# Kernel optimization log

Hardware: AMD Instinct MI355X
Metric: run time of the kernel (lower is better)

## Reference

```python
import jax, jax.numpy as jnp
from jax import lax
import numpy as np

B, T, F = 4, 16000, 512          # batch, frames, enc_num_feats
NB = 24                          # 3 stacks x 8 layers
DILS = [2 ** l for _ in range(3) for l in range(8)]


def _prelu(x, a):
    return jnp.where(x >= 0, x, a * x)


def _conv(x, w, stride=1, pad=0, dil=1, groups=1):
    # x: [B,C,T], w: [O, C//groups, K]
    return lax.conv_general_dilated(x, w, (stride,), [(pad, pad)], rhs_dilation=(dil,),
                                    dimension_numbers=('NCH', 'OIH', 'NCH'),
                                    feature_group_count=groups)


def _tconv(x, w, stride=1):
    # torch ConvTranspose1d, weight layout [in, out, k], padding=0
    k = w.shape[-1]
    wf = jnp.flip(w, -1).transpose(1, 0, 2)  # [out, in, k]
    return lax.conv_general_dilated(x, wf, (1,), [(k - 1, k - 1)], lhs_dilation=(stride,),
                                    dimension_numbers=('NCH', 'OIH', 'NCH'))


def _pw(x, w, b):
    # 1x1 conv as GEMM; w: [O,C], b: [O]
    return jnp.einsum('oc,bct->bot', w, x) + b[:, None]


def _branch(x, p):
    # encoder
    f = _conv(x, p['enc_w0'], stride=8)                       # [B,512,1999]
    f = _prelu(_conv(f, p['enc_w1']), p['enc_a'][0])          # [B,512,1997]
    f = _prelu(_conv(f, p['enc_w2']), p['enc_a'][1])          # [B,512,1995]
    # mask generator (TCN)
    o = _pw(f, p['mg_in_w'], p['mg_in_b'])                    # [B,128,t]
    for i in range(NB):
        d = DILS[i]
        h = _prelu(_pw(o, p['blk_w1'][i], p['blk_b1'][i]), p['blk_a1'][i])     # [B,32,t]
        h = _conv(h, p['blk_dw'][i][:, None, :], pad=d, dil=d, groups=32) + p['blk_db'][i][:, None]
        h = _prelu(h, p['blk_a2'][i])
        if i < NB - 1:  # last block has no residual path
            o = o + _pw(h, p['blk_rw'][i], p['blk_rb'][i])
        o = o + _pw(h, p['blk_sw'][i], p['blk_sb'][i])
    m = jax.nn.sigmoid(_pw(_prelu(o, p['mg_out_a']), p['mg_out_w'], p['mg_out_b']))  # [B,1024,t]
    b, _, t = f.shape
    m = m.reshape(b, 2, F, t)
    y = (m * f[:, None]).reshape(b * 2, F, t)
    # decoder
    y = _prelu(_tconv(y, p['dec_w1']), p['dec_a'][0])
    y = _prelu(_tconv(y, p['dec_w2']), p['dec_a'][1])
    y = _tconv(y, p['dec_w3'], stride=8)                      # [2B,1,T]
    return y.reshape(b, 2, -1)


_NAMES = ['x_real', 'x_imag', 'enc_w0', 'enc_w1', 'enc_w2', 'enc_a', 'mg_in_w', 'mg_in_b',
          'blk_w1', 'blk_b1', 'blk_a1', 'blk_dw', 'blk_db', 'blk_a2', 'blk_rw', 'blk_rb',
          'blk_sw', 'blk_sb', 'mg_out_a', 'mg_out_w', 'mg_out_b', 'dec_w1', 'dec_w2', 'dec_a', 'dec_w3']


def _forward(*args):
    p = dict(zip(_NAMES, args))
    out_r = _branch(p['x_real'], p)
    out_i = _branch(p['x_imag'], p)
    return jnp.stack([out_r, out_i])  # [2, B, 2, T]; axis0 = (real, imag)


def setup_inputs() -> dict:
    key = jax.random.key(0)
    ks = jax.random.split(key, 16)
    n = lambda k, s, sc: jax.random.normal(k, s, dtype=jnp.float32) * sc
    f32 = jnp.float32
    return {
        'x_real': jax.random.normal(ks[0], (B, 1, T), dtype=f32),
        'x_imag': jax.random.normal(ks[1], (B, 1, T), dtype=f32),
        'enc_w0': n(ks[2], (512, 1, 16), 0.1),
        'enc_w1': n(ks[3], (512, 512, 3), 0.03),
        'enc_w2': n(ks[4], (512, 512, 3), 0.03),
        'enc_a': jnp.full((2,), 0.25, f32),
        'mg_in_w': n(ks[5], (128, 512), 0.05),
        'mg_in_b': jnp.zeros((128,), f32),
        'blk_w1': n(ks[6], (NB, 32, 128), 0.08),
        'blk_b1': jnp.zeros((NB, 32), f32),
        'blk_a1': jnp.full((NB,), 0.25, f32),
        'blk_dw': n(ks[7], (NB, 32, 3), 0.2),
        'blk_db': jnp.zeros((NB, 32), f32),
        'blk_a2': jnp.full((NB,), 0.25, f32),
        'blk_rw': n(ks[8], (NB, 128, 32), 0.08),  # index NB-1 unused (no_residual)
        'blk_rb': jnp.zeros((NB, 128), f32),
        'blk_sw': n(ks[9], (NB, 128, 32), 0.08),
        'blk_sb': jnp.zeros((NB, 128), f32),
        'mg_out_a': jnp.asarray(0.25, f32),
        'mg_out_w': n(ks[10], (1024, 128), 0.08),
        'mg_out_b': jnp.zeros((1024,), f32),
        'dec_w1': n(ks[11], (512, 512, 3), 0.03),
        'dec_w2': n(ks[12], (512, 512, 3), 0.03),
        'dec_a': jnp.full((2,), 0.25, f32),
        'dec_w3': n(ks[13], (512, 1, 16), 0.1),
    }


def reference(x_real, x_imag, enc_w0, enc_w1, enc_w2, enc_a, mg_in_w, mg_in_b,
              blk_w1, blk_b1, blk_a1, blk_dw, blk_db, blk_a2, blk_rw, blk_rb,
              blk_sw, blk_sb, mg_out_a, mg_out_w, mg_out_b, dec_w1, dec_w2, dec_a, dec_w3):
    return _forward(x_real, x_imag, enc_w0, enc_w1, enc_w2, enc_a, mg_in_w, mg_in_b,
                    blk_w1, blk_b1, blk_a1, blk_dw, blk_db, blk_a2, blk_rw, blk_rb,
                    blk_sw, blk_sb, mg_out_a, mg_out_w, mg_out_b, dec_w1, dec_w2, dec_a, dec_w3)
```

## Files before the change

kernel.cpp:

```cpp
#include <hip/hip_runtime.h>
#include <hip/hip_cooperative_groups.h>

namespace cg = cooperative_groups;


typedef unsigned short u16;
typedef __attribute__((ext_vector_type(8))) short bf16x8_t;
typedef __attribute__((ext_vector_type(4))) float f32x4_t;

#define ST    2064
#define HALO  8
#define TR    2064
#define RHALO 8

#define U_F0H   0ULL
#define U_F1H   8454144ULL
#define F_F2    8454144ULL
#define F_D2    0ULL
#define U_YH    33816576ULL
#define U_D1H   50724864ULL
#define F_O     33816576ULL
#define F_G0    35930112ULL
#define F_G1    36458496ULL
#define F_W     36986880ULL
#define W_MGIN  0ULL
#define W_MGOUT 65536ULL
#define W_W1T   196608ULL
#define W_WSUMT 294912ULL
#define W_BSUM  393216ULL
#define U_WB    74766336ULL
#define F_FLAG  38956032ULL
#define F_G2    38964224ULL
#define F_G3    39492608ULL
#define U_MKB   74104832ULL
#define U_W1B   74375168ULL
#define U_WSB   74563584ULL

#define WS_HI 0
#define WS_LO 5120
#define W1_HI 10240
#define W1_LO 14592
#define OB_HI 0
#define OB_LO 8704
#define HB_HI 0
#define HB_LO 2560

__device__ __forceinline__ float prelu_f(float x, float a) { return x >= 0.f ? x : a * x; }
__device__ __forceinline__ u16 f2b(float f) {
    unsigned u = __float_as_uint(f);
    return (u16)((u + 0x7FFF + ((u >> 16) & 1)) >> 16);
}
__device__ __forceinline__ float b2f(u16 h) {
    return __uint_as_float((unsigned)h << 16);
}
__device__ __forceinline__ void gload16(const void* g, void* l) {
    __builtin_amdgcn_global_load_lds(
        (const __attribute__((address_space(1))) unsigned*)g,
        (__attribute__((address_space(3))) unsigned*)l, 16, 0, 0);
}

__global__ __launch_bounds__(256) void prep_all(
    const float* __restrict__ ew1, const float* __restrict__ ew2,
    const float* __restrict__ dw1, const float* __restrict__ dw2,
    const float* __restrict__ mgin_w, const float* __restrict__ mgout_w,
    const float* __restrict__ bw1, const float* __restrict__ brw,
    const float* __restrict__ brb, const float* __restrict__ bsw,
    const float* __restrict__ bsb, float* __restrict__ wsf, u16* __restrict__ wsb,
    unsigned* __restrict__ flags)
{
    const int task = blockIdx.y;
    const int idx  = blockIdx.x * 256 + threadIdx.x;
    const int stride = gridDim.x * 256;
    if (task < 4) {
        const float* src = (task == 0) ? ew1 : (task == 1) ? ew2 : (task == 2) ? dw1 : dw2;
        u16* dst = wsb + U_WB + (size_t)task * 786432ULL;
        const bool dec = (task >= 2);
        for (int n = idx; n < 786432; n += stride) {
            int j = n >> 18, o = (n >> 9) & 511, c = n & 511;
            float v = dec ? src[(size_t)c * 1536 + o * 3 + (2 - j)]
                          : src[(size_t)o * 1536 + c * 3 + j];
            dst[n] = f2b(v);
        }
    } else if (task == 4) {
        float* dst = wsf + F_W + W_MGIN;
        for (int n = idx; n < 65536; n += stride) {
            int o = n & 127, c = n >> 7;
            dst[n] = mgin_w[(size_t)o * 512 + c];
        }
    } else if (task == 5) {
        u16* dst = wsb + U_MKB;
        for (int n = idx; n < 262144; n += stride) {
            int C = n & 127, m = (n >> 7) & 1023, p = n >> 17;
            float v = mgout_w[(size_t)m * 128 + C];
            u16 hh = f2b(v);
            if (p) hh = f2b(v - b2f(hh));
            dst[n] = hh;
        }
    } else if (task == 6) {
        float* dstf = wsf + F_W + W_W1T;
        for (int n = idx; n < 4096; n += stride) {
            int cc = n & 31, C = n >> 5;
            dstf[n] = bw1[(size_t)cc * 128 + C];
        }
        u16* dstb = wsb + U_W1B;
        for (int n = idx; n < 188416; n += stride) {
            int C = n & 127, cgi = (n >> 7) & 31, p = (n >> 12) & 1, ii = n >> 13;
            float v = bw1[(size_t)(ii + 1) * 4096 + cgi * 128 + C];
            u16 hh = f2b(v);
            if (p) hh = f2b(v - b2f(hh));
            dstb[n] = hh;
        }
    } else if (task == 7) {
        u16* dst = wsb + U_WSB;
        for (int n = idx; n < 196608; n += stride) {
            int cc = n & 31, C = (n >> 5) & 127, p = (n >> 12) & 1, i = n >> 13;
            float v = bsw[(size_t)i * 4096 + C * 32 + cc];
            if (i < 23) v += brw[(size_t)i * 4096 + C * 32 + cc];
            u16 hh = f2b(v);
            if (p) hh = f2b(v - b2f(hh));
            dst[n] = hh;
        }
    } else if (task == 8) {
        float* dst = wsf + F_W + W_BSUM;
        for (int n = idx; n < 3072; n += stride) {
            int i = n >> 7;
            float v = bsb[n];
            if (i < 23) v += brb[n];
            dst[n] = v;
        }
    } else if (task == 9) {
        const unsigned long long uoff[4] = { U_F0H, U_F1H, U_YH, U_D1H };
        const int nbArr[4]   = { 8, 8, 16, 16 };
        const int trArr[4]   = { 1999, 1997, 1995, 1997 };
#pragma unroll
        for (int z = 0; z < 4; z++) {
            unsigned* base = (unsigned*)(wsb + uoff[z]);
            const int nb = nbArr[z], Treal = trArr[z];
            const int prcnt = TR - Treal;
            const int total = nb * prcnt * 256;
            for (int n = idx; n < total; n += stride) {
                const int col = n & 255;
                const int r   = n >> 8;
                const int bb  = r / prcnt;
                const int pr  = r % prcnt;
                const int row = (pr < RHALO) ? pr : (Treal + pr);
                base[((size_t)bb * TR + row) * 256 + col] = 0u;
            }
        }
    } else {
        for (int n = idx; n < 4096; n += stride) flags[n] = 0u;
    }
}

__global__ __launch_bounds__(256) void enc0_kernel(
    const float* __restrict__ xr, const float* __restrict__ xi,
    const float* __restrict__ w0, u16* __restrict__ f0h)
{
    const int t  = blockIdx.x * 256 + threadIdx.x;
    const int c0 = blockIdx.y * 8;
    const int b  = blockIdx.z;
    if (t >= 1999) return;
    const float* x = (b < 4) ? (xr + (size_t)b * 16000) : (xi + (size_t)(b - 4) * 16000);
    float xv[16];
    const int base = t * 8;
#pragma unroll
    for (int k = 0; k < 16; k++) xv[k] = x[base + k];
    union { u16 u[8]; uint4 v; } p;
#pragma unroll
    for (int cq = 0; cq < 8; cq++) {
        const float* w = w0 + (size_t)(c0 + cq) * 16;
        float acc = 0.f;
#pragma unroll
        for (int k = 0; k < 16; k++) acc = fmaf(xv[k], w[k], acc);
        p.u[cq] = f2b(acc);
    }
    *(uint4*)&f0h[((size_t)b * TR + RHALO + t) * 512 + c0] = p.v;
}

template <int JOFF, int OUTF32>
__global__ __launch_bounds__(256) void conv_mfma(
    const u16* __restrict__ in, u16* __restrict__ out16, float* __restrict__ out32,
    const u16* __restrict__ wM, const float* __restrict__ alpha_p, int Tout)
{
    __shared__ __align__(16) u16 smem[17408];
    u16* As = smem;
    u16* Bs = smem + 12288;
    const int tid  = threadIdx.x;
    const int t0   = blockIdx.x * 128;
    const int ob   = blockIdx.y * 128;
    const int b    = blockIdx.z;
    const int l15  = tid & 15;
    const int quad = (tid >> 4) & 3;
    const int wave = tid >> 6;
    const int wm   = (wave & 1) * 64;
    const int wn   = (wave >> 1) * 64;
    const u16* inb = in + (size_t)b * TR * 512;
    const int wvb  = wave * 1024;

    f32x4_t acc[4][4];
#pragma unroll
    for (int i = 0; i < 4; i++)
#pragma unroll
        for (int k = 0; k < 4; k++) acc[i][k] = (f32x4_t){0.f, 0.f, 0.f, 0.f};

    for (int c0 = 0; c0 < 512; c0 += 32) {
#pragma unroll
        for (int k = 0; k < 6; k++) {
            const int v = k * 256 + tid;
            const int j = v >> 9, r = (v >> 2) & 127, c = v & 3;
            const int cg = c ^ ((r >> 1) & 3);
            gload16(&wM[((size_t)(j * 512 + ob + r)) * 512 + c0 + cg * 8],
                    (char*)As + k * 4096 + wvb);
        }
#pragma unroll
        for (int k = 0; k < 2; k++) {
            const int v = k * 256 + tid;
            const int r = v >> 2, c = v & 3;
            const int cg = c ^ ((r >> 1) & 3);
            gload16(&inb[(size_t)(RHALO + t0 + JOFF + r) * 512 + c0 + cg * 8],
                    (char*)Bs + k * 4096 + wvb);
        }
        if (tid < 16) {
            const int v = 512 + tid;
            const int r = v >> 2, c = v & 3;
            const int cg = c ^ ((r >> 1) & 3);
            gload16(&inb[(size_t)(RHALO + t0 + JOFF + r) * 512 + c0 + cg * 8],
                    (char*)Bs + 8192);
        }
        __syncthreads();
#pragma unroll
        for (int j = 0; j < 3; j++) {
            bf16x8_t aw[4], bi[4];
#pragma unroll
            for (int mf = 0; mf < 4; mf++) {
                const int row = wm + mf * 16 + l15;
                const int ch  = quad ^ ((row >> 1) & 3);
                aw[mf] = *(const bf16x8_t*)&As[j * 4096 + row * 32 + ch * 8];
            }
#pragma unroll
            for (int nf = 0; nf < 4; nf++) {
                const int row = wn + nf * 16 + l15 + j;
                const int ch  = quad ^ ((row >> 1) & 3);
                bi[nf] = *(const bf16x8_t*)&Bs[row * 32 + ch * 8];
            }
#pragma unroll
            for (int mf = 0; mf < 4; mf++)
#pragma unroll
                for (int nf = 0; nf < 4; nf++) {
                    if (OUTF32)
                        acc[mf][nf] = __builtin_amdgcn_mfma_f32_16x16x32_bf16(
                            bi[nf], aw[mf], acc[mf][nf], 0, 0, 0);
                    else
                        acc[mf][nf] = __builtin_amdgcn_mfma_f32_16x16x32_bf16(
                            aw[mf], bi[nf], acc[mf][nf], 0, 0, 0);
                }
        }
        __syncthreads();
    }

    const float alpha = *alpha_p;
    if (!OUTF32) {
        u16* tile = smem;
#pragma unroll
        for (int mf = 0; mf < 4; mf++)
#pragma unroll
            for (int nf = 0; nf < 4; nf++) {
                const int t_loc = wn + nf * 16 + l15;
                const int c_loc = wm + mf * 16 + quad * 4;
                f32x4_t a = acc[mf][nf];
                ushort4 s;
                s.x = f2b(prelu_f(a.x, alpha));
                s.y = f2b(prelu_f(a.y, alpha));
                s.z = f2b(prelu_f(a.z, alpha));
                s.w = f2b(prelu_f(a.w, alpha));
                *(ushort4*)&tile[t_loc * 136 + c_loc] = s;
            }
        __syncthreads();
        for (int v = tid; v < 2048; v += 256) {
            const int row = v >> 4, seg = v & 15;
            const int t = t0 + row;
            if (t < Tout)
                *(uint4*)&out16[((size_t)b * TR + RHALO + t) * 512 + ob + seg * 8] =
                    *(const uint4*)&tile[row * 136 + seg * 8];
        }
    } else {
#pragma unroll
        for (int mf = 0; mf < 4; mf++)
#pragma unroll
            for (int nf = 0; nf < 4; nf++) {
                const int o  = ob + wm + mf * 16 + l15;
                const int tb = t0 + wn + nf * 16 + quad * 4;
                f32x4_t a = acc[mf][nf];
                float v0 = prelu_f(a.x, alpha), v1 = prelu_f(a.y, alpha);
                float v2 = prelu_f(a.z, alpha), v3 = prelu_f(a.w, alpha);
                float* p = out32 + ((size_t)(b * 512 + o)) * ST + HALO + tb;
                if (tb + 3 < Tout) {
                    *(float4*)p = make_float4(v0, v1, v2, v3);
                } else {
                    if (tb + 0 < Tout) p[0] = v0;
                    if (tb + 1 < Tout) p[1] = v1;
                    if (tb + 2 < Tout) p[2] = v2;
                    if (tb + 3 < Tout) p[3] = v3;
                }
            }
    }
}

__global__ __launch_bounds__(256) void mgin_kernel(
    const float* __restrict__ f2, float* __restrict__ o_buf, float* __restrict__ g_out,
    const float* __restrict__ wT, const float* __restrict__ bias,
    const float* __restrict__ w1T0, const float* __restrict__ b1_0,
    const float* __restrict__ a1_0)
{
    __shared__ float Bs[16][64];
    __shared__ float As[16][128];
    __shared__ float o_lds[128][64];
    const int tid = threadIdx.x;
    const int t0  = blockIdx.x * 64;
    const int b   = blockIdx.y;
    const float* f2b_ = f2 + (size_t)b * 512 * ST + HALO + t0;

    float acc[8][4];
#pragma unroll
    for (int i = 0; i < 8; i++)
#pragma unroll
        for (int k = 0; k < 4; k++) acc[i][k] = 0.f;
    const int tx = tid & 15, ty = tid >> 4;

    for (int c0 = 0; c0 < 512; c0 += 16) {
        {
            int c = tid >> 4, p = tid & 15;
            *(float4*)(&Bs[c][p * 4]) = *(const float4*)(f2b_ + (size_t)(c0 + c) * ST + p * 4);
        }
#pragma unroll
        for (int r = 0; r < 2; r++) {
            int n4 = tid + r * 256;
            int c = n4 >> 5, m4 = n4 & 31;
            *(float4*)(&As[c][m4 * 4]) = *(const float4*)(wT + (size_t)(c0 + c) * 128 + m4 * 4);
        }
        __syncthreads();
#pragma unroll 2
        for (int c = 0; c < 16; c++) {
            float4 bv = *(const float4*)(&Bs[c][tx * 4]);
            float a[8];
            *(float4*)(&a[0]) = *(const float4*)(&As[c][ty * 8]);
            *(float4*)(&a[4]) = *(const float4*)(&As[c][ty * 8 + 4]);
#pragma unroll
            for (int oi = 0; oi < 8; oi++) {
                acc[oi][0] = fmaf(a[oi], bv.x, acc[oi][0]);
                acc[oi][1] = fmaf(a[oi], bv.y, acc[oi][1]);
                acc[oi][2] = fmaf(a[oi], bv.z, acc[oi][2]);
                acc[oi][3] = fmaf(a[oi], bv.w, acc[oi][3]);
            }
        }
        __syncthreads();
    }

    const int tb = t0 + tx * 4;
#pragma unroll
    for (int oi = 0; oi < 8; oi++) {
        const int o = ty * 8 + oi;
        const float bo = bias[o];
        float vv[4];
#pragma unroll
        for (int kk = 0; kk < 4; kk++) vv[kk] = acc[oi][kk] + bo;
        *(float4*)(&o_lds[o][tx * 4]) = make_float4(vv[0], vv[1], vv[2], vv[3]);
        float* orow = o_buf + (size_t)(b * 128 + o) * ST + HALO + tb;
        if (tb + 3 < 1995) {
            *(float4*)orow = make_float4(vv[0], vv[1], vv[2], vv[3]);
        } else {
#pragma unroll
            for (int kk = 0; kk < 4; kk++)
                if (tb + kk < 1995) orow[kk] = vv[kk];
        }
    }
    __syncthreads();

    const int t = tid & 63, cg_ = tid >> 6;
    const float a1 = *a1_0;
    float acc2[8];
#pragma unroll
    for (int q = 0; q < 8; q++) acc2[q] = b1_0[cg_ * 8 + q];
    for (int C = 0; C < 128; C++) {
        const float ov = o_lds[C][t];
        const float4* wr = (const float4*)(w1T0 + (size_t)C * 32 + cg_ * 8);
        float4 w0 = wr[0], w1 = wr[1];
        acc2[0] = fmaf(w0.x, ov, acc2[0]); acc2[1] = fmaf(w0.y, ov, acc2[1]);
        acc2[2] = fmaf(w0.z, ov, acc2[2]); acc2[3] = fmaf(w0.w, ov, acc2[3]);
        acc2[4] = fmaf(w1.x, ov, acc2[4]); acc2[5] = fmaf(w1.y, ov, acc2[5]);
        acc2[6] = fmaf(w1.z, ov, acc2[6]); acc2[7] = fmaf(w1.w, ov, acc2[7]);
    }
    const int tt = t0 + t;
    if (tt < 1995) {
#pragma unroll
        for (int q = 0; q < 8; q++)
            g_out[(size_t)(b * 32 + cg_ * 8 + q) * ST + HALO + tt] = prelu_f(acc2[q], a1);
    }
}

__device__ __forceinline__ void poll_acquire(const unsigned* flags, int b, int j,
                                             int k, unsigned target)
{
    int lo = j - k; if (lo < 0) lo = 0;
    int hi = j + k; if (hi > 31) hi = 31;
    for (int n = lo; n <= hi; n++) {
        if (n == j) continue;
        const unsigned* p = flags + ((b << 5) + n) * 16;
        while (__hip_atomic_load(p, __ATOMIC_RELAXED, __HIP_MEMORY_SCOPE_AGENT) < target)
            __builtin_amdgcn_s_sleep(2);
    }
    __builtin_amdgcn_fence(__ATOMIC_ACQUIRE, "agent");
}

__device__ __forceinline__ void store_pair_agent(float* dst, int trel, float v0, float v1)
{
    if (trel + 1 < 1995) {
        unsigned long long raw =
            ((unsigned long long)__float_as_uint(v1) << 32) | __float_as_uint(v0);
        __hip_atomic_store((unsigned long long*)dst, raw,
                           __ATOMIC_RELAXED, __HIP_MEMORY_SCOPE_AGENT);
    } else if (trel < 1995) {
        __hip_atomic_store(dst, v0, __ATOMIC_RELAXED, __HIP_MEMORY_SCOPE_AGENT);
    }
}

__global__ __launch_bounds__(512) void tcn_fused(
    float* __restrict__ g0, float* __restrict__ g1,
    float* __restrict__ g2, float* __restrict__ g3,
    float* __restrict__ o_buf,
    const float* __restrict__ dw_all, const float* __restrict__ db_all,
    const float* __restrict__ a2_all,
    const u16* __restrict__ wsb16, const float* __restrict__ bsum_all,
    const u16* __restrict__ w1b16, const float* __restrict__ b1_all,
    const float* __restrict__ a1_all, unsigned* __restrict__ wflag)
{
    __shared__ __align__(16) u16  wbuf[18944];
    __shared__ __align__(16) u16  hbuf[5120];
    __shared__ __align__(16) u16  ob16[17408];
    __shared__ __align__(16) float g_lds[2][2176];
    __shared__ __align__(16) float halo_lds[8320];

    const int tid = threadIdx.x;
    const int blk = blockIdx.x;
    const int b   = blk & 7;
    const int jt  = blk >> 3;
    const int t0  = jt * 64;
    float* gbuf[4] = { g0, g1, g2, g3 };

    const int wv   = tid >> 6;
    const int l15  = tid & 15;
    const int quad = (tid >> 4) & 3;
    const int Cb   = wv * 16 + quad * 4;

    f32x4_t o_acc[4];
#pragma unroll
    for (int k = 0; k < 4; k++)
#pragma unroll
        for (int r = 0; r < 4; r++)
            o_acc[k][r] = o_buf[((size_t)(b * 128 + Cb + r)) * ST + HALO + t0 + k * 16 + l15];
    {
        int cc = tid >> 4, seg = tid & 15;
        *(float4*)&g_lds[0][cc * 68 + seg * 4] =
            *(const float4*)&g0[((size_t)(b * 32 + cc)) * ST + HALO + t0 + seg * 4];
    }

    for (int i = 0; i < 24; i++) {
        const int dil  = 1 << (i & 7);
        const int dil2 = (dil < 2) ? 2 : dil;
        const int k_rd = (dil > 64) ? 2 : 1;
        const float* gin_g = gbuf[i & 3];
        float* gout_g      = gbuf[(i + 1) & 3];
        float* gin_lds  = g_lds[i & 1];
        float* gout_lds = g_lds[(i + 1) & 1];

        {
            const u16* wsg = wsb16 + (size_t)i * 8192;
#pragma unroll
            for (int k = 0; k < 2; k++) {
                int c = tid + k * 512;
                int p = c >> 9, r = (c >> 2) & 127, s = c & 3;
                *(uint4*)&wbuf[(p ? WS_LO : WS_HI) + r * 40 + s * 8] =
                    *(const uint4*)&wsg[c * 8];
            }
            if (i < 23) {
                const u16* w1g = w1b16 + (size_t)i * 8192;
#pragma unroll
                for (int k = 0; k < 2; k++) {
                    int c = tid + k * 512;
                    int p = c >> 9, cgi = (c >> 4) & 31, s = c & 15;
                    *(uint4*)&wbuf[(p ? W1_LO : W1_HI) + cgi * 136 + s * 8] =
                        *(const uint4*)&w1g[c * 8];
                }
            }
        }

        if (i > 0 && tid == 0) poll_acquire(wflag, b, jt, k_rd, (unsigned)i);
        __syncthreads();

        {
            const int dsh = (dil2 >= 128) ? 7 : (dil2 >= 64) ? 6 : (dil2 >= 32) ? 5
                          : (dil2 >= 16) ? 4 : (dil2 >= 8) ? 3 : (dil2 >= 4) ? 2 : 1;
            const int total = 32 << dsh;
            for (int n = tid; n < total; n += 512) {
                const int cc = n >> dsh;
                const int pi = n & (dil2 - 1);
                const int hc = pi * 2;
                const int tg = (hc < dil2) ? (t0 - dil2 + hc) : (t0 + 64 + hc - dil2);
                float v0 = 0.f, v1 = 0.f;
                const float* src = gin_g + ((size_t)(b * 32 + cc)) * ST + HALO + tg;
                if (tg >= 0 && tg + 1 < 1995) {
                    unsigned long long raw = __hip_atomic_load(
                        (const unsigned long long*)src,
                        __ATOMIC_RELAXED, __HIP_MEMORY_SCOPE_AGENT);
                    v0 = __uint_as_float((unsigned)raw);
                    v1 = __uint_as_float((unsigned)(raw >> 32));
                } else {
                    if (tg >= 0 && tg < 1995)
                        v0 = __hip_atomic_load(src, __ATOMIC_RELAXED,
                                               __HIP_MEMORY_SCOPE_AGENT);
                    if (tg + 1 >= 0 && tg + 1 < 1995)
                        v1 = __hip_atomic_load(src + 1, __ATOMIC_RELAXED,
                                               __HIP_MEMORY_SCOPE_AGENT);
                }
                halo_lds[cc * 260 + hc]     = v0;
                halo_lds[cc * 260 + hc + 1] = v1;
            }
        }
        __syncthreads();

        {
            const float a2 = a2_all[i];
            const int t = tid & 63, cc0 = (tid >> 6) * 4;
            const int tt = t0 + t;
            ushort4 hi4, lo4;
            u16 hs[4], ls[4];
#pragma unroll
            for (int q = 0; q < 4; q++) {
                const int cc = cc0 + q;
                const float w0 = dw_all[i * 96 + cc * 3 + 0];
                const float w1v = dw_all[i * 96 + cc * 3 + 1];
                const float w2 = dw_all[i * 96 + cc * 3 + 2];
                const float ctr = gin_lds[cc * 68 + t];
                float lo = 0.f, hi = 0.f;
                const int tm = tt - dil;
                if (tm >= 0)
                    lo = (tm >= t0) ? gin_lds[cc * 68 + (tm - t0)]
                                    : halo_lds[cc * 260 + (tm - t0 + dil2)];
                const int tp = tt + dil;
                if (tp < 1995)
                    hi = (tp < t0 + 64) ? gin_lds[cc * 68 + (tp - t0)]
                                        : halo_lds[cc * 260 + (dil2 + tp - t0 - 64)];
                float s = db_all[i * 32 + cc] + w1v * ctr;
                s = fmaf(w0, lo, s);
                s = fmaf(w2, hi, s);
                const float hval = prelu_f(s, a2);
                const u16 hh = f2b(hval);
                hs[q] = hh;
                ls[q] = f2b(hval - b2f(hh));
            }
            hi4.x = hs[0]; hi4.y = hs[1]; hi4.z = hs[2]; hi4.w = hs[3];
            lo4.x = ls[0]; lo4.y = ls[1]; lo4.z = ls[2]; lo4.w = ls[3];
            *(ushort4*)&hbuf[HB_HI + t * 40 + cc0] = hi4;
            *(ushort4*)&hbuf[HB_LO + t * 40 + cc0] = lo4;
        }
        __syncthreads();

        {
            const bf16x8_t a_hi = *(const bf16x8_t*)&wbuf[WS_HI + (wv * 16 + l15) * 40 + quad * 8];
            const bf16x8_t a_lo = *(const bf16x8_t*)&wbuf[WS_LO + (wv * 16 + l15) * 40 + quad * 8];
            const float4 bs4 = *(const float4*)&bsum_all[i * 128 + Cb];
#pragma unroll
            for (int k = 0; k < 4; k++) {
                const bf16x8_t b_hi = *(const bf16x8_t*)&hbuf[HB_HI + (k * 16 + l15) * 40 + quad * 8];
                const bf16x8_t b_lo = *(const bf16x8_t*)&hbuf[HB_LO + (k * 16 + l15) * 40 + quad * 8];
                f32x4_t acc = o_acc[k];
                acc = __builtin_amdgcn_mfma_f32_16x16x32_bf16(a_lo, b_hi, acc, 0, 0, 0);
                acc = __builtin_amdgcn_mfma_f32_16x16x32_bf16(a_hi, b_lo, acc, 0, 0, 0);
                acc = __builtin_amdgcn_mfma_f32_16x16x32_bf16(a_hi, b_hi, acc, 0, 0, 0);
                acc.x += bs4.x; acc.y += bs4.y; acc.z += bs4.z; acc.w += bs4.w;
                o_acc[k] = acc;
            }
        }

        if (i == 23) break;

#pragma unroll
        for (int k = 0; k < 4; k++) {
            ushort4 hi4, lo4;
            u16 hs[4], ls[4];
#pragma unroll
            for (int r = 0; r < 4; r++) {
                const float v = o_acc[k][r];
                const u16 hh = f2b(v);
                hs[r] = hh;
                ls[r] = f2b(v - b2f(hh));
            }
            hi4.x = hs[0]; hi4.y = hs[1]; hi4.z = hs[2]; hi4.w = hs[3];
            lo4.x = ls[0]; lo4.y = ls[1]; lo4.z = ls[2]; lo4.w = ls[3];
            const int t_loc = k * 16 + l15;
            *(ushort4*)&ob16[OB_HI + t_loc * 136 + Cb] = hi4;
            *(ushort4*)&ob16[OB_LO + t_loc * 136 + Cb] = lo4;
        }
        __syncthreads();

        {
            const int cgb = (wv & 1) * 16;
            const int tb  = (wv >> 1) * 16;
            const float4 b14 = *(const float4*)&b1_all[(i + 1) * 32 + cgb + quad * 4];
            f32x4_t ga = (f32x4_t){b14.x, b14.y, b14.z, b14.w};
            f32x4_t gc = (f32x4_t){0.f, 0.f, 0.f, 0.f};
#pragma unroll
            for (int slab = 0; slab < 4; slab++) {
                const bf16x8_t wa_hi = *(const bf16x8_t*)&wbuf[W1_HI + (cgb + l15) * 136 + slab * 32 + quad * 8];
                const bf16x8_t wa_lo = *(const bf16x8_t*)&wbuf[W1_LO + (cgb + l15) * 136 + slab * 32 + quad * 8];
                const bf16x8_t obh   = *(const bf16x8_t*)&ob16[OB_HI + (tb + l15) * 136 + slab * 32 + quad * 8];
                const bf16x8_t obl   = *(const bf16x8_t*)&ob16[OB_LO + (tb + l15) * 136 + slab * 32 + quad * 8];
                if (slab & 1) {
                    gc = __builtin_amdgcn_mfma_f32_16x16x32_bf16(wa_lo, obh, gc, 0, 0, 0);
                    gc = __builtin_amdgcn_mfma_f32_16x16x32_bf16(wa_hi, obl, gc, 0, 0, 0);
                    gc = __builtin_amdgcn_mfma_f32_16x16x32_bf16(wa_hi, obh, gc, 0, 0, 0);
                } else {
                    ga = __builtin_amdgcn_mfma_f32_16x16x32_bf16(wa_lo, obh, ga, 0, 0, 0);
                    ga = __builtin_amdgcn_mfma_f32_16x16x32_bf16(wa_hi, obl, ga, 0, 0, 0);
                    ga = __builtin_amdgcn_mfma_f32_16x16x32_bf16(wa_hi, obh, ga, 0, 0, 0);
                }
            }
            const float a1 = a1_all[i + 1];
#pragma unroll
            for (int r = 0; r < 4; r++) {
                const int cgr = cgb + quad * 4 + r;
                gout_lds[cgr * 68 + tb + l15] = prelu_f(ga[r] + gc[r], a1);
            }
        }
        __syncthreads();

        {
            const int dnext = 1 << ((i + 1) & 7);
            int md2 = (dnext > 64) ? 64 : dnext;
            if (md2 < 2) md2 = 2;
            if (md2 >= 64) {
                for (int n = tid; n < 1024; n += 512) {
                    const int cc = n >> 5, pi = n & 31;
                    const int lt = pi * 2;
                    float* dst = gout_g + ((size_t)(b * 32 + cc)) * ST + HALO + t0 + lt;
                    store_pair_agent(dst, t0 + lt,
                                     gout_lds[cc * 68 + lt], gout_lds[cc * 68 + lt + 1]);
                }
            } else {
                const int msh = (md2 >= 32) ? 5 : (md2 >= 16) ? 4 : (md2 >= 8) ? 3
                              : (md2 >= 4) ? 2 : 1;
                const int total = 32 << msh;
                for (int n = tid; n < total; n += 512) {
                    const int cc = n >> msh;
                    const int pi = n & (md2 - 1);
                    const int hc = pi * 2;
                    const int lt = (hc < md2) ? hc : (64 - 2 * md2 + hc);
                    float* dst = gout_g + ((size_t)(b * 32 + cc)) * ST + HALO + t0 + lt;
                    store_pair_agent(dst, t0 + lt,
                                     gout_lds[cc * 68 + lt], gout_lds[cc * 68 + lt + 1]);
                }
            }
        }
        __syncthreads();

        if (tid == 0)
            __hip_atomic_store(&wflag[((b << 5) + jt) * 16], (unsigned)(i + 1),
                               __ATOMIC_RELAXED, __HIP_MEMORY_SCOPE_AGENT);
    }

#pragma unroll
    for (int k = 0; k < 4; k++)
#pragma unroll
        for (int r = 0; r < 4; r++)
            o_buf[((size_t)(b * 128 + Cb + r)) * ST + HALO + t0 + k * 16 + l15] = o_acc[k][r];
}

__global__ __launch_bounds__(256) void mask_kernel(
    const float* __restrict__ o_buf, const float* __restrict__ f2, u16* __restrict__ yh,
    const u16* __restrict__ wA, const float* __restrict__ mb,
    const float* __restrict__ a_out_p)
{
    __shared__ __align__(16) u16 smem[33792];
    u16* As = smem;
    u16* ob = smem + 16384;

    const int tid  = threadIdx.x;
    const int t0   = blockIdx.x * 64;
    const int m0   = blockIdx.y * 256;
    const int b    = blockIdx.z;
    const float ao = *a_out_p;
    const int l15  = tid & 15;
    const int quad = (tid >> 4) & 3;
    const int wave = tid >> 6;
    const int wm   = wave * 64;

    {
        const int C = tid >> 1, th = (tid & 1) * 32;
        const float* orow = o_buf + (size_t)(b * 128 + C) * ST + HALO + t0 + th;
#pragma unroll
        for (int q = 0; q < 8; q++) {
            float4 v = *(const float4*)(orow + q * 4);
            const float vv[4] = {v.x, v.y, v.z, v.w};
#pragma unroll
            for (int j = 0; j < 4; j++) {
                const float pv = prelu_f(vv[j], ao);
                const u16 hh = f2b(pv);
                const int t = th + q * 4 + j;
                ob[OB_HI + t * 136 + C] = hh;
                ob[OB_LO + t * 136 + C] = f2b(pv - b2f(hh));
            }
        }
    }

    f32x4_t acc[4][4];
#pragma unroll
    for (int mf = 0; mf < 4; mf++)
#pragma unroll
        for (int nf = 0; nf < 4; nf++) acc[mf][nf] = (f32x4_t){0.f, 0.f, 0.f, 0.f};

    for (int ks = 0; ks < 4; ks++) {
#pragma unroll
        for (int k = 0; k < 8; k++) {
            const int v = k * 256 + tid;
            const int p = v >> 10, r = (v >> 2) & 255, c = v & 3;
            const int cg = c ^ ((r >> 1) & 3);
            gload16(&wA[(size_t)p * 131072 + (size_t)(m0 + r) * 128 + ks * 32 + cg * 8],
                    (char*)As + k * 4096 + wave * 1024);
        }
        __syncthreads();
        bf16x8_t ah[4], al[4], bh[4], bl[4];
#pragma unroll
        for (int mf = 0; mf < 4; mf++) {
            const int row = wm + mf * 16 + l15;
            const int ch  = quad ^ ((row >> 1) & 3);
            ah[mf] = *(const bf16x8_t*)&As[row * 32 + ch * 8];
            al[mf] = *(const bf16x8_t*)&As[8192 + row * 32 + ch * 8];
        }
#pragma unroll
        for (int nf = 0; nf < 4; nf++) {
            const int rt = nf * 16 + l15;
            bh[nf] = *(const bf16x8_t*)&ob[OB_HI + rt * 136 + ks * 32 + quad * 8];
            bl[nf] = *(const bf16x8_t*)&ob[OB_LO + rt * 136 + ks * 32 + quad * 8];
        }
#pragma unroll
        for (int mf = 0; mf < 4; mf++)
#pragma unroll
            for (int nf = 0; nf < 4; nf++) {
                acc[mf][nf] = __builtin_amdgcn_mfma_f32_16x16x32_bf16(al[mf], bh[nf], acc[mf][nf], 0, 0, 0);
                acc[mf][nf] = __builtin_amdgcn_mfma_f32_16x16x32_bf16(ah[mf], bl[nf], acc[mf][nf], 0, 0, 0);
                acc[mf][nf] = __builtin_amdgcn_mfma_f32_16x16x32_bf16(ah[mf], bh[nf], acc[mf][nf], 0, 0, 0);
            }
        __syncthreads();
    }

    const int F0 = m0 & 511, sIdx = m0 >> 9;
    u16* tile = smem;
#pragma unroll
    for (int mf = 0; mf < 4; mf++)
#pragma unroll
        for (int nf = 0; nf < 4; nf++) {
            const int tl = nf * 16 + l15;
            u16 sv[4];
#pragma unroll
            for (int r = 0; r < 4; r++) {
                const int mloc = wm + mf * 16 + quad * 4 + r;
                const float x = acc[mf][nf][r] + mb[m0 + mloc];
                const float mval = 1.f / (1.f + __expf(-x));
                const float y = mval *
                    f2[(size_t)(b * 512 + F0 + mloc) * ST + HALO + t0 + tl];
                sv[r] = f2b(y);
            }
            ushort4 s;
            s.x = sv[0]; s.y = sv[1]; s.z = sv[2]; s.w = sv[3];
            *(ushort4*)&tile[tl * 264 + wm + mf * 16 + quad * 4] = s;
        }
    __syncthreads();
    u16* ybase = yh + ((size_t)(b * 2 + sIdx) * TR) * 512;
    for (int v = tid; v < 2048; v += 256) {
        const int row = v >> 5, seg = v & 31;
        const int t = t0 + row;
        if (t < 1995)
            *(uint4*)&ybase[(size_t)(RHALO + t) * 512 + F0 + seg * 8] =
                *(const uint4*)&tile[row * 264 + seg * 8];
    }
}

__global__ __launch_bounds__(256) void dec3_kernel(
    const float* __restrict__ d2, const float* __restrict__ w3, float* __restrict__ out)
{
    __shared__ float tile[512][34];
    const int tid = threadIdx.x;
    const int bb  = blockIdx.y;
    const int tau0 = blockIdx.x * 256;
    const int tbase = (tau0 >> 3) - 1;
    const float* src = d2 + (size_t)bb * 512 * ST + HALO + tbase;
    for (int n = tid; n < 512 * 34; n += 256) {
        int o = n / 34, i = n % 34;
        const int tg = tbase + i;
        tile[o][i] = (tg >= 0 && tg < 1999) ? src[(size_t)o * ST + i] : 0.f;
    }
    __syncthreads();

    const int tau = tau0 + tid;
    if (tau >= 16000) return;
    const int k1 = tau & 7;
    const int t1l = (tid >> 3) + 1;
    float acc = 0.f;
#pragma unroll 8
    for (int o = 0; o < 512; o++) {
        acc = fmaf(tile[o][t1l],     w3[o * 16 + k1],     acc);
        acc = fmaf(tile[o][t1l - 1], w3[o * 16 + 8 + k1], acc);
    }
    const int p = bb >> 1, s = bb & 1;
    out[(size_t)(p * 2 + s) * 16000 + tau] = acc;
}

extern "C" void kernel_launch(void* const* d_in, const int* in_sizes, int n_in,
                              void* d_out, int out_size, void* d_ws, size_t ws_size,
                              hipStream_t stream)
{
    (void)in_sizes; (void)n_in; (void)out_size; (void)ws_size;
    float* ws  = (float*)d_ws;
    u16*   wsu = (u16*)d_ws;
    const float* x_real   = (const float*)d_in[0];
    const float* x_imag   = (const float*)d_in[1];
    const float* enc_w0   = (const float*)d_in[2];
    const float* enc_w1   = (const float*)d_in[3];
    const float* enc_w2   = (const float*)d_in[4];
    const float* enc_a    = (const float*)d_in[5];
    const float* mg_in_w  = (const float*)d_in[6];
    const float* mg_in_b  = (const float*)d_in[7];
    const float* blk_w1   = (const float*)d_in[8];
    const float* blk_b1   = (const float*)d_in[9];
    const float* blk_a1   = (const float*)d_in[10];
    const float* blk_dw   = (const float*)d_in[11];
    const float* blk_db   = (const float*)d_in[12];
    const float* blk_a2   = (const float*)d_in[13];
    const float* blk_rw   = (const float*)d_in[14];
    const float* blk_rb   = (const float*)d_in[15];
    const float* blk_sw   = (const float*)d_in[16];
    const float* blk_sb   = (const float*)d_in[17];
    const float* mg_out_a = (const float*)d_in[18];
    const float* mg_out_w = (const float*)d_in[19];
    const float* mg_out_b = (const float*)d_in[20];
    const float* dec_w1   = (const float*)d_in[21];
    const float* dec_w2   = (const float*)d_in[22];
    const float* dec_a    = (const float*)d_in[23];
    const float* dec_w3   = (const float*)d_in[24];
    float* out = (float*)d_out;

    u16*   f0h   = wsu + U_F0H;
    u16*   f1h   = wsu + U_F1H;
    float* f2    = ws  + F_F2;
    float* d2    = ws  + F_D2;
    u16*   yh    = wsu + U_YH;
    u16*   d1h   = wsu + U_D1H;
    float* obuf  = ws  + F_O;
    float* g0    = ws  + F_G0;
    float* g1    = ws  + F_G1;
    float* g2    = ws  + F_G2;
    float* g3    = ws  + F_G3;
    float* WF    = ws  + F_W;
    u16*   WB    = wsu + U_WB;
    unsigned* flags = (unsigned*)(ws + F_FLAG);

    const dim3 blk(256);

    prep_all<<<dim3(64, 11), blk, 0, stream>>>(enc_w1, enc_w2, dec_w1, dec_w2,
        mg_in_w, mg_out_w, blk_w1, blk_rw, blk_rb, blk_sw, blk_sb, ws, wsu, flags);

    enc0_kernel<<<dim3(8, 64, 8), blk, 0, stream>>>(x_real, x_imag, enc_w0, f0h);

    conv_mfma<0, 0><<<dim3(16, 4, 8), blk, 0, stream>>>(
        f0h, f1h, nullptr, WB + 0 * 786432, enc_a + 0, 1997);
    conv_mfma<0, 1><<<dim3(16, 4, 8), blk, 0, stream>>>(
        f1h, nullptr, f2, WB + 1 * 786432, enc_a + 1, 1995);

    mgin_kernel<<<dim3(32, 8), blk, 0, stream>>>(f2, obuf, g0, WF + W_MGIN, mg_in_b,
        WF + W_W1T, blk_b1, blk_a1);

    {
        const float* dwp   = blk_dw;
        const float* dbp   = blk_db;
        const float* a2p   = blk_a2;
        const u16*   wsbp  = wsu + U_WSB;
        const float* bsump = WF + W_BSUM;
        const u16*   w1bp  = wsu + U_W1B;
        const float* b1p   = blk_b1;
        const float* a1p   = blk_a1;
        unsigned* flg = flags;
        void* args[] = { &g0, &g1, &g2, &g3, &obuf,
                         (void*)&dwp, (void*)&dbp, (void*)&a2p,
                         (void*)&wsbp, (void*)&bsump, (void*)&w1bp,
                         (void*)&b1p, (void*)&a1p, &flg };
        (void)hipLaunchCooperativeKernel((void*)tcn_fused, dim3(256), dim3(512),
                                         args, 0, stream);
    }

    mask_kernel<<<dim3(32, 4, 8), blk, 0, stream>>>(obuf, f2, yh,
        wsu + U_MKB, mg_out_b, mg_out_a);

    conv_mfma<-2, 0><<<dim3(16, 4, 16), blk, 0, stream>>>(
        yh, d1h, nullptr, WB + 2 * 786432, dec_a + 0, 1997);
    conv_mfma<-2, 1><<<dim3(16, 4, 16), blk, 0, stream>>>(
        d1h, nullptr, d2, WB + 3 * 786432, dec_a + 1, 1999);

    dec3_kernel<<<dim3(63, 16), blk, 0, stream>>>(d2, dec_w3, out);
}
```

Baseline: 715.0 us.

## Move mask-gen input projection to split-bf16 MFMA and halve encoder conv time tile

The mgin 512->128 pointwise GEMM changes from a scalar FP32 FMA tiling to MFMA bf16 instructions. It keeps accuracy by splitting both weights and activations into hi/lo bf16 parts and using three MFMAs per tile. The weights are pre-split in the prep kernel, and activations are split on the fly into LDS. Separately, the encoder conv kernels get a TT=64 time tile that doubles the grid, aimed at better CU occupancy for the batch-8 encoder launches. The trade-off is extra conversion work, and the triple-MFMA bf16 emulation may differ numerically from FP32.

```diff
diff --git a/kernel.cpp b/kernel.cpp
--- a/kernel.cpp
+++ b/kernel.cpp
@@ -32,6 +32,7 @@
 #define F_FLAG  38956032ULL
 #define F_G2    38964224ULL
 #define F_G3    39492608ULL
+#define U_MGB   73973760ULL
 #define U_MKB   74104832ULL
 #define U_W1B   74375168ULL
 #define U_WSB   74563584ULL
@@ -82,10 +83,13 @@
             dst[n] = f2b(v);
         }
     } else if (task == 4) {
-        float* dst = wsf + F_W + W_MGIN;
-        for (int n = idx; n < 65536; n += stride) {
-            int o = n & 127, c = n >> 7;
-            dst[n] = mgin_w[(size_t)o * 512 + c];
+        u16* dst = wsb + U_MGB;
+        for (int n = idx; n < 131072; n += stride) {
+            int C = n & 511, m = (n >> 9) & 127, p = n >> 16;
+            float v = mgin_w[(size_t)m * 512 + C];
+            u16 hh = f2b(v);
+            if (p) hh = f2b(v - b2f(hh));
+            dst[n] = hh;
         }
     } else if (task == 5) {
         u16* dst = wsb + U_MKB;
@@ -177,31 +181,34 @@
     *(uint4*)&f0h[((size_t)b * TR + RHALO + t) * 512 + c0] = p.v;
 }
 
-template <int JOFF, int OUTF32>
+template <int JOFF, int OUTF32, int TT>
 __global__ __launch_bounds__(256) void conv_mfma(
     const u16* __restrict__ in, u16* __restrict__ out16, float* __restrict__ out32,
     const u16* __restrict__ wM, const float* __restrict__ alpha_p, int Tout)
 {
-    __shared__ __align__(16) u16 smem[17408];
+    constexpr int NF    = TT / 32;
+    constexpr int BFULL = TT / 64;
+    constexpr int SMEMSZ = (TT == 128) ? 17408 : 14464;
+    __shared__ __align__(16) u16 smem[SMEMSZ];
     u16* As = smem;
     u16* Bs = smem + 12288;
     const int tid  = threadIdx.x;
-    const int t0   = blockIdx.x * 128;
+    const int t0   = blockIdx.x * TT;
     const int ob   = blockIdx.y * 128;
     const int b    = blockIdx.z;
     const int l15  = tid & 15;
     const int quad = (tid >> 4) & 3;
     const int wave = tid >> 6;
     const int wm   = (wave & 1) * 64;
-    const int wn   = (wave >> 1) * 64;
+    const int wn   = (wave >> 1) * (TT / 2);
     const u16* inb = in + (size_t)b * TR * 512;
     const int wvb  = wave * 1024;
 
-    f32x4_t acc[4][4];
+    f32x4_t acc[4][NF];
 #pragma unroll
     for (int i = 0; i < 4; i++)
 #pragma unroll
-        for (int k = 0; k < 4; k++) acc[i][k] = (f32x4_t){0.f, 0.f, 0.f, 0.f};
+        for (int k = 0; k < NF; k++) acc[i][k] = (f32x4_t){0.f, 0.f, 0.f, 0.f};
 
     for (int c0 = 0; c0 < 512; c0 += 32) {
 #pragma unroll
@@ -213,7 +220,7 @@
                     (char*)As + k * 4096 + wvb);
         }
 #pragma unroll
-        for (int k = 0; k < 2; k++) {
+        for (int k = 0; k < BFULL; k++) {
             const int v = k * 256 + tid;
             const int r = v >> 2, c = v & 3;
             const int cg = c ^ ((r >> 1) & 3);
@@ -221,16 +228,16 @@
                     (char*)Bs + k * 4096 + wvb);
         }
         if (tid < 16) {
-            const int v = 512 + tid;
+            const int v = BFULL * 256 + tid;
             const int r = v >> 2, c = v & 3;
             const int cg = c ^ ((r >> 1) & 3);
             gload16(&inb[(size_t)(RHALO + t0 + JOFF + r) * 512 + c0 + cg * 8],
-                    (char*)Bs + 8192);
+                    (char*)Bs + BFULL * 4096);
         }
         __syncthreads();
 #pragma unroll
         for (int j = 0; j < 3; j++) {
-            bf16x8_t aw[4], bi[4];
+            bf16x8_t aw[4], bi[NF];
 #pragma unroll
             for (int mf = 0; mf < 4; mf++) {
                 const int row = wm + mf * 16 + l15;
@@ -238,7 +245,7 @@
                 aw[mf] = *(const bf16x8_t*)&As[j * 4096 + row * 32 + ch * 8];
             }
 #pragma unroll
-            for (int nf = 0; nf < 4; nf++) {
+            for (int nf = 0; nf < NF; nf++) {
                 const int row = wn + nf * 16 + l15 + j;
                 const int ch  = quad ^ ((row >> 1) & 3);
                 bi[nf] = *(const bf16x8_t*)&Bs[row * 32 + ch * 8];
@@ -246,7 +253,7 @@
 #pragma unroll
             for (int mf = 0; mf < 4; mf++)
 #pragma unroll
-                for (int nf = 0; nf < 4; nf++) {
+                for (int nf = 0; nf < NF; nf++) {
                     if (OUTF32)
                         acc[mf][nf] = __builtin_amdgcn_mfma_f32_16x16x32_bf16(
                             bi[nf], aw[mf], acc[mf][nf], 0, 0, 0);
@@ -264,7 +271,7 @@
 #pragma unroll
         for (int mf = 0; mf < 4; mf++)
 #pragma unroll
-            for (int nf = 0; nf < 4; nf++) {
+            for (int nf = 0; nf < NF; nf++) {
                 const int t_loc = wn + nf * 16 + l15;
                 const int c_loc = wm + mf * 16 + quad * 4;
                 f32x4_t a = acc[mf][nf];
@@ -276,7 +283,7 @@
                 *(ushort4*)&tile[t_loc * 136 + c_loc] = s;
             }
         __syncthreads();
-        for (int v = tid; v < 2048; v += 256) {
+        for (int v = tid; v < TT * 16; v += 256) {
             const int row = v >> 4, seg = v & 15;
             const int t = t0 + row;
             if (t < Tout)
@@ -287,7 +294,7 @@
 #pragma unroll
         for (int mf = 0; mf < 4; mf++)
 #pragma unroll
-            for (int nf = 0; nf < 4; nf++) {
+            for (int nf = 0; nf < NF; nf++) {
                 const int o  = ob + wm + mf * 16 + l15;
                 const int tb = t0 + wn + nf * 16 + quad * 4;
                 f32x4_t a = acc[mf][nf];
@@ -308,73 +315,100 @@
 
 __global__ __launch_bounds__(256) void mgin_kernel(
     const float* __restrict__ f2, float* __restrict__ o_buf, float* __restrict__ g_out,
-    const float* __restrict__ wT, const float* __restrict__ bias,
+    const u16* __restrict__ wA, const float* __restrict__ bias,
     const float* __restrict__ w1T0, const float* __restrict__ b1_0,
     const float* __restrict__ a1_0)
 {
-    __shared__ float Bs[16][64];
-    __shared__ float As[16][128];
-    __shared__ float o_lds[128][64];
+    __shared__ __align__(16) u16   As[8192];
+    __shared__ __align__(16) u16   Bsm[5120];
+    __shared__ __align__(16) float o_lds[128 * 68];
     const int tid = threadIdx.x;
     const int t0  = blockIdx.x * 64;
     const int b   = blockIdx.y;
-    const float* f2b_ = f2 + (size_t)b * 512 * ST + HALO + t0;
-
-    float acc[8][4];
-#pragma unroll
-    for (int i = 0; i < 8; i++)
-#pragma unroll
-        for (int k = 0; k < 4; k++) acc[i][k] = 0.f;
-    const int tx = tid & 15, ty = tid >> 4;
-
-    for (int c0 = 0; c0 < 512; c0 += 16) {
+    const int l15 = tid & 15, quad = (tid >> 4) & 3, wave = tid >> 6;
+    const int wm  = wave * 32;
+    const int bc  = tid >> 3;
+    const int bs  = tid & 7;
+
+    f32x4_t acc[2][4];
+#pragma unroll
+    for (int mf = 0; mf < 2; mf++)
+#pragma unroll
+        for (int nf = 0; nf < 4; nf++) acc[mf][nf] = (f32x4_t){0.f, 0.f, 0.f, 0.f};
+
+    for (int ks = 0; ks < 16; ks++) {
+#pragma unroll
+        for (int k = 0; k < 4; k++) {
+            const int v = k * 256 + tid;
+            const int p = v >> 9, r = (v >> 2) & 127, c = v & 3;
+            const int cg = c ^ ((r >> 1) & 3);
+            gload16(&wA[(size_t)p * 65536 + (size_t)r * 512 + ks * 32 + cg * 8],
+                    (char*)As + k * 4096 + wave * 1024);
+        }
         {
-            int c = tid >> 4, p = tid & 15;
-            *(float4*)(&Bs[c][p * 4]) = *(const float4*)(f2b_ + (size_t)(c0 + c) * ST + p * 4);
-        }
-#pragma unroll
-        for (int r = 0; r < 2; r++) {
-            int n4 = tid + r * 256;
-            int c = n4 >> 5, m4 = n4 & 31;
-            *(float4*)(&As[c][m4 * 4]) = *(const float4*)(wT + (size_t)(c0 + c) * 128 + m4 * 4);
-        }
-        __syncthreads();
-#pragma unroll 2
-        for (int c = 0; c < 16; c++) {
-            float4 bv = *(const float4*)(&Bs[c][tx * 4]);
-            float a[8];
-            *(float4*)(&a[0]) = *(const float4*)(&As[c][ty * 8]);
-            *(float4*)(&a[4]) = *(const float4*)(&As[c][ty * 8 + 4]);
-#pragma unroll
-            for (int oi = 0; oi < 8; oi++) {
-                acc[oi][0] = fmaf(a[oi], bv.x, acc[oi][0]);
-                acc[oi][1] = fmaf(a[oi], bv.y, acc[oi][1]);
-                acc[oi][2] = fmaf(a[oi], bv.z, acc[oi][2]);
-                acc[oi][3] = fmaf(a[oi], bv.w, acc[oi][3]);
-            }
-        }
-        __syncthreads();
-    }
-
-    const int tb = t0 + tx * 4;
-#pragma unroll
-    for (int oi = 0; oi < 8; oi++) {
-        const int o = ty * 8 + oi;
-        const float bo = bias[o];
-        float vv[4];
-#pragma unroll
-        for (int kk = 0; kk < 4; kk++) vv[kk] = acc[oi][kk] + bo;
-        *(float4*)(&o_lds[o][tx * 4]) = make_float4(vv[0], vv[1], vv[2], vv[3]);
-        float* orow = o_buf + (size_t)(b * 128 + o) * ST + HALO + tb;
+            const float* src = f2 + (size_t)(b * 512 + ks * 32 + bc) * ST + HALO + t0 + bs * 8;
+            float4 v0 = *(const float4*)src;
+            float4 v1 = *(const float4*)(src + 4);
+            const float vv[8] = {v0.x, v0.y, v0.z, v0.w, v1.x, v1.y, v1.z, v1.w};
+#pragma unroll
+            for (int j = 0; j < 8; j++) {
+                const int t = bs * 8 + j;
+                const u16 hh = f2b(vv[j]);
+                Bsm[t * 40 + bc] = hh;
+                Bsm[2560 + t * 40 + bc] = f2b(vv[j] - b2f(hh));
+            }
+        }
+        __syncthreads();
+        bf16x8_t ah[2], al[2], bh[4], bl[4];
+#pragma unroll
+        for (int mf = 0; mf < 2; mf++) {
+            const int row = wm + mf * 16 + l15;
+            const int ch  = quad ^ ((row >> 1) & 3);
+            ah[mf] = *(const bf16x8_t*)&As[row * 32 + ch * 8];
+            al[mf] = *(const bf16x8_t*)&As[4096 + row * 32 + ch * 8];
+        }
+#pragma unroll
+        for (int nf = 0; nf < 4; nf++) {
+            const int rt = nf * 16 + l15;
+            bh[nf] = *(const bf16x8_t*)&Bsm[rt * 40 + quad * 8];
+            bl[nf] = *(const bf16x8_t*)&Bsm[2560 + rt * 40 + quad * 8];
+        }
+#pragma unroll
+        for (int mf = 0; mf < 2; mf++)
+#pragma unroll
+            for (int nf = 0; nf < 4; nf++) {
+                acc[mf][nf] = __builtin_amdgcn_mfma_f32_16x16x32_bf16(al[mf], bh[nf], acc[mf][nf], 0, 0, 0);
+                acc[mf][nf] = __builtin_amdgcn_mfma_f32_16x16x32_bf16(ah[mf], bl[nf], acc[mf][nf], 0, 0, 0);
+                acc[mf][nf] = __builtin_amdgcn_mfma_f32_16x16x32_bf16(ah[mf], bh[nf], acc[mf][nf], 0, 0, 0);
+            }
+        __syncthreads();
+    }
+
+#pragma unroll
+    for (int mf = 0; mf < 2; mf++)
+#pragma unroll
+        for (int nf = 0; nf < 4; nf++) {
+#pragma unroll
+            for (int r = 0; r < 4; r++) {
+                const int m = wm + mf * 16 + quad * 4 + r;
+                o_lds[m * 68 + nf * 16 + l15] = acc[mf][nf][r] + bias[m];
+            }
+        }
+    __syncthreads();
+
+    for (int n = tid; n < 2048; n += 256) {
+        const int row = n >> 4, seg = n & 15;
+        const int tb = t0 + seg * 4;
+        float* dst = o_buf + (size_t)(b * 128 + row) * ST + HALO + tb;
+        const float* srcl = &o_lds[row * 68 + seg * 4];
         if (tb + 3 < 1995) {
-            *(float4*)orow = make_float4(vv[0], vv[1], vv[2], vv[3]);
+            *(float4*)dst = *(const float4*)srcl;
         } else {
 #pragma unroll
             for (int kk = 0; kk < 4; kk++)
-                if (tb + kk < 1995) orow[kk] = vv[kk];
-        }
-    }
-    __syncthreads();
+                if (tb + kk < 1995) dst[kk] = srcl[kk];
+        }
+    }
 
     const int t = tid & 63, cg_ = tid >> 6;
     const float a1 = *a1_0;
@@ -382,7 +416,7 @@
 #pragma unroll
     for (int q = 0; q < 8; q++) acc2[q] = b1_0[cg_ * 8 + q];
     for (int C = 0; C < 128; C++) {
-        const float ov = o_lds[C][t];
+        const float ov = o_lds[C * 68 + t];
         const float4* wr = (const float4*)(w1T0 + (size_t)C * 32 + cg_ * 8);
         float4 w0 = wr[0], w1 = wr[1];
         acc2[0] = fmaf(w0.x, ov, acc2[0]); acc2[1] = fmaf(w0.y, ov, acc2[1]);
@@ -871,12 +905,12 @@
 
     enc0_kernel<<<dim3(8, 64, 8), blk, 0, stream>>>(x_real, x_imag, enc_w0, f0h);
 
-    conv_mfma<0, 0><<<dim3(16, 4, 8), blk, 0, stream>>>(
+    conv_mfma<0, 0, 64><<<dim3(32, 4, 8), blk, 0, stream>>>(
         f0h, f1h, nullptr, WB + 0 * 786432, enc_a + 0, 1997);
-    conv_mfma<0, 1><<<dim3(16, 4, 8), blk, 0, stream>>>(
+    conv_mfma<0, 1, 64><<<dim3(32, 4, 8), blk, 0, stream>>>(
         f1h, nullptr, f2, WB + 1 * 786432, enc_a + 1, 1995);
 
-    mgin_kernel<<<dim3(32, 8), blk, 0, stream>>>(f2, obuf, g0, WF + W_MGIN, mg_in_b,
+    mgin_kernel<<<dim3(32, 8), blk, 0, stream>>>(f2, obuf, g0, wsu + U_MGB, mg_in_b,
         WF + W_W1T, blk_b1, blk_a1);
 
     {
@@ -900,9 +934,9 @@
     mask_kernel<<<dim3(32, 4, 8), blk, 0, stream>>>(obuf, f2, yh,
         wsu + U_MKB, mg_out_b, mg_out_a);
 
-    conv_mfma<-2, 0><<<dim3(16, 4, 16), blk, 0, stream>>>(
+    conv_mfma<-2, 0, 128><<<dim3(16, 4, 16), blk, 0, stream>>>(
         yh, d1h, nullptr, WB + 2 * 786432, dec_a + 0, 1997);
-    conv_mfma<-2, 1><<<dim3(16, 4, 16), blk, 0, stream>>>(
+    conv_mfma<-2, 1, 128><<<dim3(16, 4, 16), blk, 0, stream>>>(
         d1h, nullptr, d2, WB + 3 * 786432, dec_a + 1, 1999);
 
     dec3_kernel<<<dim3(63, 16), blk, 0, stream>>>(d2, dec_w3, out);
```

New measurement: 708.7 us, median of 3. Within noise of the previous version (-0.9%).
